# Optimization experiments

Hardware: AMD Instinct MI355X
Metric: run time of the kernel (lower is better)

The kernel has to match this reference:

```python
import jax, jax.numpy as jnp
import numpy as np

# dims (match init_kwargs / input_specs)
R, C, HD, D, K = 16, 64, 4, 16, 4   # num_rims, channels_per_rim, num_heads, depth, top_k
B, H, W = 8, 64, 64


def setup_inputs() -> dict:
    key = jax.random.key(0)
    ks = jax.random.split(key, 12)
    s = 0.02  # small init scale like torch conv default-ish
    OC = R * HD * D  # 1024
    return {
        "x":    jax.random.normal(ks[0], (B, C, H, W), jnp.float32),
        "rims": jax.random.normal(ks[1], (R, C), jnp.float32) * 0.01,  # spatial 1x1 squeezed
        "Wk":   jax.random.normal(ks[2], (OC, C), jnp.float32) * s,
        "bk":   jax.random.normal(ks[3], (OC,), jnp.float32) * s,
        "Wv":   jax.random.normal(ks[4], (OC, C), jnp.float32) * s,
        "bv":   jax.random.normal(ks[5], (OC,), jnp.float32) * s,
        "Wq":   jax.random.normal(ks[6], (OC, C), jnp.float32) * s,   # grouped conv, groups=R: (R, HD*D, C)
        "bq":   jax.random.normal(ks[7], (OC,), jnp.float32) * s,
        "Wm":   jax.random.normal(ks[8], (R * C, HD * D), jnp.float32) * s,  # merge heads, groups=R
        "bm":   jax.random.normal(ks[9], (R * C,), jnp.float32) * s,
        "Wo":   jax.random.normal(ks[10], (C, C), jnp.float32) * s,
        "bo":   jax.random.normal(ks[11], (C,), jnp.float32) * s,
    }


def reference(x, rims, Wk, bk, Wv, bv, Wq, bq, Wm, bm, Wo, bo):
    Bx, _, Hx, Wx = x.shape
    # input_key: cat(x, zeros) along batch, then 1x1 conv + relu -> [2B, R*HD*D, H, W]
    x2 = jnp.concatenate([x, jnp.zeros_like(x)], axis=0)
    keyf = jax.nn.relu(jnp.einsum('bchw,oc->bohw', x2, Wk) + bk[:, None, None])
    # input_value: 1x1 conv + relu -> [B, R*HD*D, H, W]
    val = jax.nn.relu(jnp.einsum('bchw,oc->bohw', x, Wv) + bv[:, None, None])
    # rims_query: grouped 1x1 conv over rims template -> [R, HD, D]
    q = jax.nn.relu(jnp.einsum('rc,rdc->rd', rims, Wq.reshape(R, HD * D, C))
                    + bq.reshape(R, HD * D)).reshape(R, HD, D)
    # attention inner product: grouped 1x1 conv (groups=R*HD) == per-(rim,head) dot over depth
    ip = jnp.einsum('brhdxy,rhd->brhxy', keyf.reshape(2 * Bx, R, HD, D, Hx, Wx), q)
    # softmax over the real-vs-null pair (dim 0 after split)
    attn = jax.nn.softmax(ip.reshape(2, Bx, R, HD, Hx, Wx), axis=0)
    attn_sum = attn.sum(axis=3)                 # [2, B, R, H, W]
    scores = jnp.moveaxis(attn_sum[0], 1, -1)   # [B, H, W, R]
    _, idx = jax.lax.top_k(scores, K)           # [B, H, W, K] (sorted)
    # merge heads: grouped 1x1 conv (groups=R) -> [B, R, C, H, W]
    merged = jnp.einsum('brdhw,rcd->brchw', val.reshape(Bx, R, HD * D, Hx, Wx),
                        Wm.reshape(R, C, HD * D)) \
             + bm.reshape(R, C)[None, :, :, None, None]
    # gather top-k rims per pixel, then mean over k
    idx2 = jnp.transpose(idx, (0, 3, 1, 2))[:, :, None, :, :]   # [B, K, 1, H, W]
    gathered = jnp.take_along_axis(merged, idx2, axis=1)        # [B, K, C, H, W]
    out = gathered.mean(axis=1)                                 # dropout(eval) = identity
    out = jax.nn.relu(out)
    # out projection: 1x1 conv + relu
    out = jax.nn.relu(jnp.einsum('bchw,oc->bohw', out, Wo) + bo[:, None, None])
    return out
```

## Files before the change

### kernel.cpp

```cpp
#include <hip/hip_runtime.h>
#include <math.h>

#define RN   16
#define CN   64
#define HDN  4
#define DN   16
#define KN   4
#define HWN  4096
#define NPIX 32768
#define OCN  1024
#define CHW  (CN*HWN)

__global__ __launch_bounds__(256) void rims_fused(
    const float* __restrict__ x,   const float* __restrict__ rims,
    const float* __restrict__ Wk,  const float* __restrict__ bk,
    const float* __restrict__ Wv,  const float* __restrict__ bv,
    const float* __restrict__ Wq,  const float* __restrict__ bq,
    const float* __restrict__ Wm,  const float* __restrict__ bm,
    const float* __restrict__ Wo,  const float* __restrict__ bo,
    float* __restrict__ out)
{
  __shared__ float q_s[OCN];
  __shared__ float ipn_s[64];
  __shared__ float sc_s[16 * 65];
  __shared__ float macc_s[64 * 65];
  __shared__ int   bcnt[16];
  __shared__ int   bpos[16];
  __shared__ unsigned char brim[256];
  __shared__ unsigned char bpix[256];

  const int tid   = threadIdx.x;
  const int tile  = blockIdx.x;
  const int b     = tile >> 6;
  const int pbase = (tile & 63) * 64;
  const float* xbase = x + (size_t)b * CHW + pbase;

  for (int o = tid; o < OCN; o += 256) {
    const int r = o >> 6;
    const float* wq = Wq + o * CN;
    const float* rp = rims + r * CN;
    float a0 = bq[o], a1 = 0.f, a2 = 0.f, a3 = 0.f;
    #pragma unroll
    for (int c = 0; c < CN; c += 4) {
      a0 = fmaf(wq[c+0], rp[c+0], a0);
      a1 = fmaf(wq[c+1], rp[c+1], a1);
      a2 = fmaf(wq[c+2], rp[c+2], a2);
      a3 = fmaf(wq[c+3], rp[c+3], a3);
    }
    q_s[o] = fmaxf((a0 + a1) + (a2 + a3), 0.f);
  }
  __syncthreads();
  if (tid < 64) {
    float acc = 0.f;
    #pragma unroll
    for (int d = 0; d < DN; ++d)
      acc = fmaf(fmaxf(bk[tid * DN + d], 0.f), q_s[tid * DN + d], acc);
    ipn_s[tid] = acc;
  }
  __syncthreads();

  {
    const int pl = tid & 63;
    const int g  = tid >> 6;
    const float* xp = xbase + pl;
    float xv[CN];
    #pragma unroll
    for (int c = 0; c < CN; ++c) xv[c] = xp[c * HWN];

    #pragma unroll 1
    for (int rr = 0; rr < 4; ++rr) {
      const int r = g * 4 + rr;
      float score = 0.f;
      #pragma unroll 1
      for (int h = 0; h < HDN; ++h) {
        const int rh = r * HDN + h;
        float qrow[DN];
        #pragma unroll
        for (int d = 0; d < DN; ++d) qrow[d] = q_s[rh * DN + d];
        const float ipn = ipn_s[rh];
        float ip = 0.f;
        #pragma unroll 1
        for (int d = 0; d < DN; ++d) {
          const float qv = qrow[d];
          if (qv != 0.f) {
            const int o = rh * DN + d;
            const float* w = Wk + o * CN;
            float a0 = bk[o], a1 = 0.f, a2 = 0.f, a3 = 0.f;
            #pragma unroll
            for (int c = 0; c < CN; c += 4) {
              a0 = fmaf(w[c+0], xv[c+0], a0);
              a1 = fmaf(w[c+1], xv[c+1], a1);
              a2 = fmaf(w[c+2], xv[c+2], a2);
              a3 = fmaf(w[c+3], xv[c+3], a3);
            }
            ip = fmaf(fmaxf((a0 + a1) + (a2 + a3), 0.f), qv, ip);
          }
        }
        score += 1.f / (1.f + expf(ipn - ip));
      }
      sc_s[r * 65 + pl] = score;
    }
  }
  __syncthreads();

  for (int i = tid; i < 64 * 65; i += 256) macc_s[i] = 0.f;
  if (tid < 16) bcnt[tid] = 0;
  __syncthreads();

  int rs0 = 0, rs1 = 0, rs2 = 0, rs3 = 0;
  if (tid < 64) {
    float s[RN];
    #pragma unroll
    for (int r = 0; r < RN; ++r) s[r] = sc_s[r * 65 + tid];
    #pragma unroll
    for (int k = 0; k < KN; ++k) {
      float best = -3.4e38f; int bi = 0;
      #pragma unroll
      for (int r = 0; r < RN; ++r) { if (s[r] > best) { best = s[r]; bi = r; } }
      if (k == 0) rs0 = bi; else if (k == 1) rs1 = bi;
      else if (k == 2) rs2 = bi; else rs3 = bi;
      s[bi] = -3.4e38f;
    }
    atomicAdd(&bcnt[rs0], 1); atomicAdd(&bcnt[rs1], 1);
    atomicAdd(&bcnt[rs2], 1); atomicAdd(&bcnt[rs3], 1);
  }
  __syncthreads();
  if (tid == 0) {
    int run = 0;
    #pragma unroll
    for (int r = 0; r < RN; ++r) { bpos[r] = run; run += bcnt[r]; }
  }
  __syncthreads();
  if (tid < 64) {
    int p0 = atomicAdd(&bpos[rs0], 1); brim[p0] = (unsigned char)rs0; bpix[p0] = (unsigned char)tid;
    int p1 = atomicAdd(&bpos[rs1], 1); brim[p1] = (unsigned char)rs1; bpix[p1] = (unsigned char)tid;
    int p2 = atomicAdd(&bpos[rs2], 1); brim[p2] = (unsigned char)rs2; bpix[p2] = (unsigned char)tid;
    int p3 = atomicAdd(&bpos[rs3], 1); brim[p3] = (unsigned char)rs3; bpix[p3] = (unsigned char)tid;
  }
  __syncthreads();

  {
    const int rim = (int)brim[tid];
    const int pp  = (int)bpix[tid];
    const float* xp = xbase + pp;
    float xv[CN];
    #pragma unroll
    for (int c = 0; c < CN; ++c) xv[c] = xp[c * HWN];

    float macc[CN];
    const float* bmp = bm + rim * CN;
    #pragma unroll
    for (int c = 0; c < CN; ++c) macc[c] = bmp[c];

    const float* wvb = Wv + (size_t)(rim * 64) * CN;
    const float* bvp = bv + rim * 64;
    const float* wmb = Wm + (size_t)(rim * CN) * 64;

    #pragma unroll 1
    for (int d0 = 0; d0 < 64; d0 += 8) {
      float vald[8];
      #pragma unroll
      for (int k8 = 0; k8 < 8; ++k8) {
        const int d = d0 + k8;
        const float* w = wvb + d * CN;
        float a0 = bvp[d], a1 = 0.f, a2 = 0.f, a3 = 0.f;
        #pragma unroll
        for (int c = 0; c < CN; c += 4) {
          a0 = fmaf(w[c+0], xv[c+0], a0);
          a1 = fmaf(w[c+1], xv[c+1], a1);
          a2 = fmaf(w[c+2], xv[c+2], a2);
          a3 = fmaf(w[c+3], xv[c+3], a3);
        }
        vald[k8] = fmaxf((a0 + a1) + (a2 + a3), 0.f);
      }
      #pragma unroll
      for (int c = 0; c < CN; ++c) {
        const float* wm = wmb + c * 64 + d0;
        float m = macc[c];
        #pragma unroll
        for (int k8 = 0; k8 < 8; ++k8) m = fmaf(wm[k8], vald[k8], m);
        macc[c] = m;
      }
    }
    #pragma unroll
    for (int c = 0; c < CN; ++c)
      atomicAdd(&macc_s[pp * 65 + c], macc[c]);
  }
  __syncthreads();

  {
    const int j  = tid >> 6;
    const int pl = tid & 63;
    float u[CN];
    #pragma unroll
    for (int c = 0; c < CN; ++c)
      u[c] = fmaxf(macc_s[pl * 65 + c] * 0.25f, 0.f);
    float* op = out + (size_t)b * CHW + pbase + pl;
    #pragma unroll 1
    for (int t = 0; t < 16; ++t) {
      const int co = j * 16 + t;
      const float* w = Wo + co * CN;
      float a0 = bo[co], a1 = 0.f, a2 = 0.f, a3 = 0.f;
      #pragma unroll
      for (int c = 0; c < CN; c += 4) {
        a0 = fmaf(w[c+0], u[c+0], a0);
        a1 = fmaf(w[c+1], u[c+1], a1);
        a2 = fmaf(w[c+2], u[c+2], a2);
        a3 = fmaf(w[c+3], u[c+3], a3);
      }
      op[co * HWN] = fmaxf((a0 + a1) + (a2 + a3), 0.f);
    }
  }
}

extern "C" void kernel_launch(void* const* d_in, const int* in_sizes, int n_in,
                              void* d_out, int out_size, void* d_ws, size_t ws_size,
                              hipStream_t stream) {
  (void)in_sizes; (void)n_in; (void)d_ws; (void)ws_size; (void)out_size;
  const float* xx   = (const float*)d_in[0];
  const float* rims = (const float*)d_in[1];
  const float* Wk   = (const float*)d_in[2];
  const float* bk   = (const float*)d_in[3];
  const float* Wv   = (const float*)d_in[4];
  const float* bv   = (const float*)d_in[5];
  const float* Wq   = (const float*)d_in[6];
  const float* bq   = (const float*)d_in[7];
  const float* Wm   = (const float*)d_in[8];
  const float* bm   = (const float*)d_in[9];
  const float* Wo   = (const float*)d_in[10];
  const float* bo   = (const float*)d_in[11];
  float* outp = (float*)d_out;

  rims_fused<<<dim3(NPIX / 64), dim3(256), 0, stream>>>(
      xx, rims, Wk, bk, Wv, bv, Wq, bq, Wm, bm, Wo, bo, outp);
}
```

Before: 398.3 us.

## Double block to 512 threads, compact active key channels, split merge work per pair

```diff
diff --git a/kernel.cpp b/kernel.cpp
--- a/kernel.cpp
+++ b/kernel.cpp
@@ -11,7 +11,7 @@
 #define OCN  1024
 #define CHW  (CN*HWN)
 
-__global__ __launch_bounds__(256) void rims_fused(
+__global__ __launch_bounds__(512, 4) void rims_fused(
     const float* __restrict__ x,   const float* __restrict__ rims,
     const float* __restrict__ Wk,  const float* __restrict__ bk,
     const float* __restrict__ Wv,  const float* __restrict__ bv,
@@ -22,6 +22,9 @@
 {
   __shared__ float q_s[OCN];
   __shared__ float ipn_s[64];
+  __shared__ float act_qv[64][16];
+  __shared__ int   act_o[64][16];
+  __shared__ int   act_cnt[64];
   __shared__ float sc_s[16 * 65];
   __shared__ float macc_s[64 * 65];
   __shared__ int   bcnt[16];
@@ -35,7 +38,17 @@
   const int pbase = (tile & 63) * 64;
   const float* xbase = x + (size_t)b * CHW + pbase;
 
-  for (int o = tid; o < OCN; o += 256) {
+  const int pl = tid & 63;
+  const int wv = tid >> 6;
+
+  float xv[CN];
+  {
+    const float* xp = xbase + pl;
+    #pragma unroll
+    for (int c = 0; c < CN; ++c) xv[c] = xp[c * HWN];
+  }
+
+  for (int o = tid; o < OCN; o += 512) {
     const int r = o >> 6;
     const float* wq = Wq + o * CN;
     const float* rp = rims + r * CN;
@@ -51,119 +64,35 @@
   }
   __syncthreads();
   if (tid < 64) {
-    float acc = 0.f;
-    #pragma unroll
-    for (int d = 0; d < DN; ++d)
-      acc = fmaf(fmaxf(bk[tid * DN + d], 0.f), q_s[tid * DN + d], acc);
-    ipn_s[tid] = acc;
-  }
-  __syncthreads();
-
-  {
-    const int pl = tid & 63;
-    const int g  = tid >> 6;
-    const float* xp = xbase + pl;
-    float xv[CN];
-    #pragma unroll
-    for (int c = 0; c < CN; ++c) xv[c] = xp[c * HWN];
-
+    int cnt = 0; float acc = 0.f;
+    #pragma unroll
+    for (int d = 0; d < DN; ++d) {
+      const int o = tid * DN + d;
+      const float qv = q_s[o];
+      acc = fmaf(fmaxf(bk[o], 0.f), qv, acc);
+      if (qv != 0.f) { act_o[tid][cnt] = o; act_qv[tid][cnt] = qv; ++cnt; }
+    }
+    ipn_s[tid]   = acc;
+    act_cnt[tid] = cnt;
+  }
+  __syncthreads();
+
+  #pragma unroll 1
+  for (int rr = 0; rr < 2; ++rr) {
+    const int r = wv * 2 + rr;
+    float score = 0.f;
     #pragma unroll 1
-    for (int rr = 0; rr < 4; ++rr) {
-      const int r = g * 4 + rr;
-      float score = 0.f;
-      #pragma unroll 1
-      for (int h = 0; h < HDN; ++h) {
-        const int rh = r * HDN + h;
-        float qrow[DN];
-        #pragma unroll
-        for (int d = 0; d < DN; ++d) qrow[d] = q_s[rh * DN + d];
-        const float ipn = ipn_s[rh];
-        float ip = 0.f;
-        #pragma unroll 1
-        for (int d = 0; d < DN; ++d) {
-          const float qv = qrow[d];
-          if (qv != 0.f) {
-            const int o = rh * DN + d;
-            const float* w = Wk + o * CN;
-            float a0 = bk[o], a1 = 0.f, a2 = 0.f, a3 = 0.f;
-            #pragma unroll
-            for (int c = 0; c < CN; c += 4) {
-              a0 = fmaf(w[c+0], xv[c+0], a0);
-              a1 = fmaf(w[c+1], xv[c+1], a1);
-              a2 = fmaf(w[c+2], xv[c+2], a2);
-              a3 = fmaf(w[c+3], xv[c+3], a3);
-            }
-            ip = fmaf(fmaxf((a0 + a1) + (a2 + a3), 0.f), qv, ip);
-          }
-        }
-        score += 1.f / (1.f + expf(ipn - ip));
-      }
-      sc_s[r * 65 + pl] = score;
-    }
-  }
-  __syncthreads();
-
-  for (int i = tid; i < 64 * 65; i += 256) macc_s[i] = 0.f;
-  if (tid < 16) bcnt[tid] = 0;
-  __syncthreads();
-
-  int rs0 = 0, rs1 = 0, rs2 = 0, rs3 = 0;
-  if (tid < 64) {
-    float s[RN];
-    #pragma unroll
-    for (int r = 0; r < RN; ++r) s[r] = sc_s[r * 65 + tid];
-    #pragma unroll
-    for (int k = 0; k < KN; ++k) {
-      float best = -3.4e38f; int bi = 0;
-      #pragma unroll
-      for (int r = 0; r < RN; ++r) { if (s[r] > best) { best = s[r]; bi = r; } }
-      if (k == 0) rs0 = bi; else if (k == 1) rs1 = bi;
-      else if (k == 2) rs2 = bi; else rs3 = bi;
-      s[bi] = -3.4e38f;
-    }
-    atomicAdd(&bcnt[rs0], 1); atomicAdd(&bcnt[rs1], 1);
-    atomicAdd(&bcnt[rs2], 1); atomicAdd(&bcnt[rs3], 1);
-  }
-  __syncthreads();
-  if (tid == 0) {
-    int run = 0;
-    #pragma unroll
-    for (int r = 0; r < RN; ++r) { bpos[r] = run; run += bcnt[r]; }
-  }
-  __syncthreads();
-  if (tid < 64) {
-    int p0 = atomicAdd(&bpos[rs0], 1); brim[p0] = (unsigned char)rs0; bpix[p0] = (unsigned char)tid;
-    int p1 = atomicAdd(&bpos[rs1], 1); brim[p1] = (unsigned char)rs1; bpix[p1] = (unsigned char)tid;
-    int p2 = atomicAdd(&bpos[rs2], 1); brim[p2] = (unsigned char)rs2; bpix[p2] = (unsigned char)tid;
-    int p3 = atomicAdd(&bpos[rs3], 1); brim[p3] = (unsigned char)rs3; bpix[p3] = (unsigned char)tid;
-  }
-  __syncthreads();
-
-  {
-    const int rim = (int)brim[tid];
-    const int pp  = (int)bpix[tid];
-    const float* xp = xbase + pp;
-    float xv[CN];
-    #pragma unroll
-    for (int c = 0; c < CN; ++c) xv[c] = xp[c * HWN];
-
-    float macc[CN];
-    const float* bmp = bm + rim * CN;
-    #pragma unroll
-    for (int c = 0; c < CN; ++c) macc[c] = bmp[c];
-
-    const float* wvb = Wv + (size_t)(rim * 64) * CN;
-    const float* bvp = bv + rim * 64;
-    const float* wmb = Wm + (size_t)(rim * CN) * 64;
-
-    #pragma unroll 1
-    for (int d0 = 0; d0 < 64; d0 += 8) {
-      float vald[8];
-      #pragma unroll
-      for (int k8 = 0; k8 < 8; ++k8) {
-        const int d = d0 + k8;
-        const float* w = wvb + d * CN;
-        float a0 = bvp[d], a1 = 0.f, a2 = 0.f, a3 = 0.f;
+    for (int h = 0; h < HDN; ++h) {
+      const int rh  = r * HDN + h;
+      const int cnt = __builtin_amdgcn_readfirstlane(act_cnt[rh]);
+      const float ipn = ipn_s[rh];
+      float ip = 0.f;
+      #pragma unroll 2
+      for (int i = 0; i < cnt; ++i) {
+        const int   o  = __builtin_amdgcn_readfirstlane(act_o[rh][i]);
+        const float qv = act_qv[rh][i];
+        const float* w = Wk + o * CN;
+        float a0 = bk[o], a1 = 0.f, a2 = 0.f, a3 = 0.f;
         #pragma unroll
         for (int c = 0; c < CN; c += 4) {
           a0 = fmaf(w[c+0], xv[c+0], a0);
@@ -171,34 +100,110 @@
           a2 = fmaf(w[c+2], xv[c+2], a2);
           a3 = fmaf(w[c+3], xv[c+3], a3);
         }
-        vald[k8] = fmaxf((a0 + a1) + (a2 + a3), 0.f);
-      }
-      #pragma unroll
-      for (int c = 0; c < CN; ++c) {
-        const float* wm = wmb + c * 64 + d0;
-        float m = macc[c];
-        #pragma unroll
-        for (int k8 = 0; k8 < 8; ++k8) m = fmaf(wm[k8], vald[k8], m);
-        macc[c] = m;
-      }
-    }
-    #pragma unroll
-    for (int c = 0; c < CN; ++c)
-      atomicAdd(&macc_s[pp * 65 + c], macc[c]);
+        ip = fmaf(fmaxf((a0 + a1) + (a2 + a3), 0.f), qv, ip);
+      }
+      score += 1.f / (1.f + expf(ipn - ip));
+    }
+    sc_s[r * 65 + pl] = score;
+  }
+  __syncthreads();
+
+  for (int i = tid; i < 64 * 65; i += 512) macc_s[i] = 0.f;
+  if (tid < 16) bcnt[tid] = 0;
+  __syncthreads();
+
+  int rs0 = 0, rs1 = 0, rs2 = 0, rs3 = 0;
+  if (tid < 64) {
+    float s[RN];
+    #pragma unroll
+    for (int r = 0; r < RN; ++r) s[r] = sc_s[r * 65 + tid];
+    #pragma unroll
+    for (int k = 0; k < KN; ++k) {
+      float best = -3.4e38f; int bi = 0;
+      #pragma unroll
+      for (int r = 0; r < RN; ++r) { if (s[r] > best) { best = s[r]; bi = r; } }
+      if (k == 0) rs0 = bi; else if (k == 1) rs1 = bi;
+      else if (k == 2) rs2 = bi; else rs3 = bi;
+      s[bi] = -3.4e38f;
+    }
+    atomicAdd(&bcnt[rs0], 1); atomicAdd(&bcnt[rs1], 1);
+    atomicAdd(&bcnt[rs2], 1); atomicAdd(&bcnt[rs3], 1);
+  }
+  __syncthreads();
+  if (tid == 0) {
+    int run = 0;
+    #pragma unroll
+    for (int r = 0; r < RN; ++r) { bpos[r] = run; run += bcnt[r]; }
+  }
+  __syncthreads();
+  if (tid < 64) {
+    int p0 = atomicAdd(&bpos[rs0], 1); brim[p0] = (unsigned char)rs0; bpix[p0] = (unsigned char)tid;
+    int p1 = atomicAdd(&bpos[rs1], 1); brim[p1] = (unsigned char)rs1; bpix[p1] = (unsigned char)tid;
+    int p2 = atomicAdd(&bpos[rs2], 1); brim[p2] = (unsigned char)rs2; bpix[p2] = (unsigned char)tid;
+    int p3 = atomicAdd(&bpos[rs3], 1); brim[p3] = (unsigned char)rs3; bpix[p3] = (unsigned char)tid;
   }
   __syncthreads();
 
   {
-    const int j  = tid >> 6;
-    const int pl = tid & 63;
+    const int e    = tid >> 1;
+    const int half = tid & 1;
+    const int rim  = (int)brim[e];
+    const int pp   = (int)bpix[e];
+    const float* xp = xbase + pp;
+    float xw[CN];
+    #pragma unroll
+    for (int c = 0; c < CN; ++c) xw[c] = xp[c * HWN];
+
+    float vald[32];
+    const float* wvb = Wv + (size_t)(rim * CN + half * 32) * CN;
+    const float* bvp = bv + rim * CN + half * 32;
+    #pragma unroll 4
+    for (int d = 0; d < 32; ++d) {
+      const float4* w4 = (const float4*)(wvb + d * CN);
+      float a0 = bvp[d], a1 = 0.f, a2 = 0.f, a3 = 0.f;
+      #pragma unroll
+      for (int c4 = 0; c4 < 16; ++c4) {
+        const float4 wq = w4[c4];
+        a0 = fmaf(wq.x, xw[c4*4+0], a0);
+        a1 = fmaf(wq.y, xw[c4*4+1], a1);
+        a2 = fmaf(wq.z, xw[c4*4+2], a2);
+        a3 = fmaf(wq.w, xw[c4*4+3], a3);
+      }
+      vald[d] = fmaxf((a0 + a1) + (a2 + a3), 0.f);
+    }
+
+    const float* wmb = Wm + (size_t)rim * CN * 64 + half * 32;
+    const float* bmp = bm + rim * CN;
+    #pragma unroll 2
+    for (int c = 0; c < CN; ++c) {
+      const float4* w4 = (const float4*)(wmb + c * 64);
+      float m0 = (half == 0) ? bmp[c] : 0.f;
+      float m1 = 0.f, m2 = 0.f, m3 = 0.f;
+      #pragma unroll
+      for (int k4 = 0; k4 < 8; ++k4) {
+        const float4 wq = w4[k4];
+        m0 = fmaf(wq.x, vald[k4*4+0], m0);
+        m1 = fmaf(wq.y, vald[k4*4+1], m1);
+        m2 = fmaf(wq.z, vald[k4*4+2], m2);
+        m3 = fmaf(wq.w, vald[k4*4+3], m3);
+      }
+      float m = (m0 + m1) + (m2 + m3);
+      m += __shfl_xor(m, 1);
+      if ((c >> 5) == half)
+        atomicAdd(&macc_s[pp * 65 + c], m);
+    }
+  }
+  __syncthreads();
+
+  {
     float u[CN];
     #pragma unroll
     for (int c = 0; c < CN; ++c)
       u[c] = fmaxf(macc_s[pl * 65 + c] * 0.25f, 0.f);
     float* op = out + (size_t)b * CHW + pbase + pl;
     #pragma unroll 1
-    for (int t = 0; t < 16; ++t) {
-      const int co = j * 16 + t;
+    for (int t = 0; t < 8; ++t) {
+      const int co = wv * 8 + t;
       const float* w = Wo + co * CN;
       float a0 = bo[co], a1 = 0.f, a2 = 0.f, a3 = 0.f;
       #pragma unroll
@@ -231,6 +236,6 @@
   const float* bo   = (const float*)d_in[11];
   float* outp = (float*)d_out;
 
-  rims_fused<<<dim3(NPIX / 64), dim3(256), 0, stream>>>(
+  rims_fused<<<dim3(NPIX / 64), dim3(512), 0, stream>>>(
       xx, rims, Wk, bk, Wv, bv, Wq, bq, Wm, bm, Wo, bo, outp);
 }
```

After: 631.3 us. 58.5% more time.

## Split fused RIMs kernel into score, mask, per-rim accumulate, and output kernels

Applied to the files above, without the earlier changes.

```diff
diff --git a/kernel.cpp b/kernel.cpp
--- a/kernel.cpp
+++ b/kernel.cpp
@@ -11,32 +11,40 @@
 #define OCN  1024
 #define CHW  (CN*HWN)
 
-__global__ __launch_bounds__(256) void rims_fused(
+#define WS_SC_BYTES   (16 * NPIX * 4)
+#define WS_MASK_BYTES (NPIX * 4)
+
+__global__ __launch_bounds__(256) void k_scores(
     const float* __restrict__ x,   const float* __restrict__ rims,
     const float* __restrict__ Wk,  const float* __restrict__ bk,
-    const float* __restrict__ Wv,  const float* __restrict__ bv,
     const float* __restrict__ Wq,  const float* __restrict__ bq,
-    const float* __restrict__ Wm,  const float* __restrict__ bm,
-    const float* __restrict__ Wo,  const float* __restrict__ bo,
-    float* __restrict__ out)
-{
-  __shared__ float q_s[OCN];
-  __shared__ float ipn_s[64];
-  __shared__ float sc_s[16 * 65];
-  __shared__ float macc_s[64 * 65];
-  __shared__ int   bcnt[16];
-  __shared__ int   bpos[16];
-  __shared__ unsigned char brim[256];
-  __shared__ unsigned char bpix[256];
-
-  const int tid   = threadIdx.x;
-  const int tile  = blockIdx.x;
-  const int b     = tile >> 6;
-  const int pbase = (tile & 63) * 64;
+    float* __restrict__ sc)
+{
+  __shared__ float q_s[512];
+  __shared__ float ipn_s[32];
+
+  const int tid  = threadIdx.x;
+  const int blk  = blockIdx.x;
+  const int T    = blk >> 1;
+  const int half = blk & 1;
+  const int b     = T >> 6;
+  const int pbase = (T & 63) * 64;
   const float* xbase = x + (size_t)b * CHW + pbase;
 
-  for (int o = tid; o < OCN; o += 256) {
-    const int r = o >> 6;
+  const int pl = tid & 63;
+  const int wv = tid >> 6;
+
+  float xv[CN];
+  {
+    const float* xp = xbase + pl;
+    #pragma unroll
+    for (int c = 0; c < CN; ++c) xv[c] = xp[c * HWN];
+  }
+
+  for (int i = 0; i < 2; ++i) {
+    const int ol = i * 256 + tid;
+    const int o  = half * 512 + ol;
+    const int r  = o >> 6;
     const float* wq = Wq + o * CN;
     const float* rp = rims + r * CN;
     float a0 = bq[o], a1 = 0.f, a2 = 0.f, a3 = 0.f;
@@ -47,129 +55,147 @@
       a2 = fmaf(wq[c+2], rp[c+2], a2);
       a3 = fmaf(wq[c+3], rp[c+3], a3);
     }
-    q_s[o] = fmaxf((a0 + a1) + (a2 + a3), 0.f);
-  }
-  __syncthreads();
-  if (tid < 64) {
+    q_s[ol] = fmaxf((a0 + a1) + (a2 + a3), 0.f);
+  }
+  __syncthreads();
+  if (tid < 32) {
     float acc = 0.f;
+    const int rh = half * 32 + tid;
     #pragma unroll
     for (int d = 0; d < DN; ++d)
-      acc = fmaf(fmaxf(bk[tid * DN + d], 0.f), q_s[tid * DN + d], acc);
+      acc = fmaf(fmaxf(bk[rh * DN + d], 0.f), q_s[tid * DN + d], acc);
     ipn_s[tid] = acc;
   }
   __syncthreads();
 
-  {
-    const int pl = tid & 63;
-    const int g  = tid >> 6;
-    const float* xp = xbase + pl;
-    float xv[CN];
-    #pragma unroll
-    for (int c = 0; c < CN; ++c) xv[c] = xp[c * HWN];
-
+  #pragma unroll 1
+  for (int rr = 0; rr < 2; ++rr) {
+    const int rl = wv * 2 + rr;
+    const int r  = half * 8 + rl;
+    float score = 0.f;
     #pragma unroll 1
-    for (int rr = 0; rr < 4; ++rr) {
-      const int r = g * 4 + rr;
-      float score = 0.f;
-      #pragma unroll 1
-      for (int h = 0; h < HDN; ++h) {
-        const int rh = r * HDN + h;
-        float qrow[DN];
-        #pragma unroll
-        for (int d = 0; d < DN; ++d) qrow[d] = q_s[rh * DN + d];
-        const float ipn = ipn_s[rh];
-        float ip = 0.f;
-        #pragma unroll 1
-        for (int d = 0; d < DN; ++d) {
-          const float qv = qrow[d];
-          if (qv != 0.f) {
-            const int o = rh * DN + d;
-            const float* w = Wk + o * CN;
-            float a0 = bk[o], a1 = 0.f, a2 = 0.f, a3 = 0.f;
-            #pragma unroll
-            for (int c = 0; c < CN; c += 4) {
-              a0 = fmaf(w[c+0], xv[c+0], a0);
-              a1 = fmaf(w[c+1], xv[c+1], a1);
-              a2 = fmaf(w[c+2], xv[c+2], a2);
-              a3 = fmaf(w[c+3], xv[c+3], a3);
-            }
-            ip = fmaf(fmaxf((a0 + a1) + (a2 + a3), 0.f), qv, ip);
-          }
-        }
-        score += 1.f / (1.f + expf(ipn - ip));
-      }
-      sc_s[r * 65 + pl] = score;
-    }
-  }
-  __syncthreads();
-
-  for (int i = tid; i < 64 * 65; i += 256) macc_s[i] = 0.f;
-  if (tid < 16) bcnt[tid] = 0;
-  __syncthreads();
-
-  int rs0 = 0, rs1 = 0, rs2 = 0, rs3 = 0;
-  if (tid < 64) {
-    float s[RN];
-    #pragma unroll
-    for (int r = 0; r < RN; ++r) s[r] = sc_s[r * 65 + tid];
-    #pragma unroll
-    for (int k = 0; k < KN; ++k) {
-      float best = -3.4e38f; int bi = 0;
-      #pragma unroll
-      for (int r = 0; r < RN; ++r) { if (s[r] > best) { best = s[r]; bi = r; } }
-      if (k == 0) rs0 = bi; else if (k == 1) rs1 = bi;
-      else if (k == 2) rs2 = bi; else rs3 = bi;
-      s[bi] = -3.4e38f;
-    }
-    atomicAdd(&bcnt[rs0], 1); atomicAdd(&bcnt[rs1], 1);
-    atomicAdd(&bcnt[rs2], 1); atomicAdd(&bcnt[rs3], 1);
-  }
-  __syncthreads();
-  if (tid == 0) {
-    int run = 0;
-    #pragma unroll
-    for (int r = 0; r < RN; ++r) { bpos[r] = run; run += bcnt[r]; }
-  }
-  __syncthreads();
-  if (tid < 64) {
-    int p0 = atomicAdd(&bpos[rs0], 1); brim[p0] = (unsigned char)rs0; bpix[p0] = (unsigned char)tid;
-    int p1 = atomicAdd(&bpos[rs1], 1); brim[p1] = (unsigned char)rs1; bpix[p1] = (unsigned char)tid;
-    int p2 = atomicAdd(&bpos[rs2], 1); brim[p2] = (unsigned char)rs2; bpix[p2] = (unsigned char)tid;
-    int p3 = atomicAdd(&bpos[rs3], 1); brim[p3] = (unsigned char)rs3; bpix[p3] = (unsigned char)tid;
-  }
-  __syncthreads();
-
-  {
-    const int rim = (int)brim[tid];
-    const int pp  = (int)bpix[tid];
-    const float* xp = xbase + pp;
-    float xv[CN];
-    #pragma unroll
-    for (int c = 0; c < CN; ++c) xv[c] = xp[c * HWN];
-
-    float macc[CN];
-    const float* bmp = bm + rim * CN;
-    #pragma unroll
-    for (int c = 0; c < CN; ++c) macc[c] = bmp[c];
-
-    const float* wvb = Wv + (size_t)(rim * 64) * CN;
-    const float* bvp = bv + rim * 64;
-    const float* wmb = Wm + (size_t)(rim * CN) * 64;
-
-    #pragma unroll 1
-    for (int d0 = 0; d0 < 64; d0 += 8) {
-      float vald[8];
-      #pragma unroll
-      for (int k8 = 0; k8 < 8; ++k8) {
-        const int d = d0 + k8;
-        const float* w = wvb + d * CN;
-        float a0 = bvp[d], a1 = 0.f, a2 = 0.f, a3 = 0.f;
+    for (int h = 0; h < HDN; ++h) {
+      const int rhl  = rl * HDN + h;
+      const int rh_u = __builtin_amdgcn_readfirstlane(r * HDN + h);
+      const float ipn = ipn_s[rhl];
+      float ip = 0.f;
+      #pragma unroll 4
+      for (int d = 0; d < DN; ++d) {
+        const float qv = q_s[rhl * DN + d];
+        const int   o  = rh_u * DN + d;
+        const float* w = Wk + o * CN;
+        float a0 = bk[o], a1 = 0.f, a2 = 0.f, a3 = 0.f;
         #pragma unroll
         for (int c = 0; c < CN; c += 4) {
           a0 = fmaf(w[c+0], xv[c+0], a0);
           a1 = fmaf(w[c+1], xv[c+1], a1);
           a2 = fmaf(w[c+2], xv[c+2], a2);
           a3 = fmaf(w[c+3], xv[c+3], a3);
+        }
+        ip = fmaf(fmaxf((a0 + a1) + (a2 + a3), 0.f), qv, ip);
+      }
+      score += 1.f / (1.f + expf(ipn - ip));
+    }
+    sc[r * NPIX + T * 64 + pl] = score;
+  }
+}
+
+__global__ __launch_bounds__(256) void k_mask(
+    const float* __restrict__ sc, unsigned int* __restrict__ mask,
+    float4* __restrict__ U4)
+{
+  const int pix = blockIdx.x * 256 + threadIdx.x;
+  for (int i = pix; i < (CN * NPIX) / 4; i += NPIX)
+    U4[i] = make_float4(0.f, 0.f, 0.f, 0.f);
+
+  float s[RN];
+  #pragma unroll
+  for (int r = 0; r < RN; ++r) s[r] = sc[r * NPIX + pix];
+  unsigned int m = 0;
+  #pragma unroll
+  for (int k = 0; k < KN; ++k) {
+    float best = -3.4e38f; int bi = 0;
+    #pragma unroll
+    for (int r = 0; r < RN; ++r) { if (s[r] > best) { best = s[r]; bi = r; } }
+    m |= (1u << bi);
+    s[bi] = -3.4e38f;
+  }
+  mask[pix] = m;
+}
+
+__global__ __launch_bounds__(256) void k_rimacc(
+    const float* __restrict__ x,  const unsigned int* __restrict__ mask,
+    const float* __restrict__ Wv, const float* __restrict__ bv,
+    const float* __restrict__ Wm, const float* __restrict__ bm,
+    float* __restrict__ U)
+{
+  __shared__ unsigned short plist[512];
+  __shared__ int wcnt[8];
+  __shared__ int woff[9];
+
+  const int tid   = threadIdx.x;
+  const int rim   = blockIdx.x >> 6;
+  const int chunk = blockIdx.x & 63;
+  const int pix0  = chunk * 512;
+  const int b     = pix0 >> 12;
+  const int hw0   = pix0 & 4095;
+  const float* xb = x + (size_t)b * CHW + hw0;
+
+  const int lane = tid & 63;
+  const int w    = tid >> 6;
+  const int i0 = w * 64 + lane;
+  const int i1 = 256 + w * 64 + lane;
+  const bool s0 = (mask[pix0 + i0] >> rim) & 1u;
+  const bool s1 = (mask[pix0 + i1] >> rim) & 1u;
+  const unsigned long long v0 = __ballot(s0);
+  const unsigned long long v1 = __ballot(s1);
+  if (lane == 0) { wcnt[w] = __popcll(v0); wcnt[4 + w] = __popcll(v1); }
+  __syncthreads();
+  if (tid == 0) {
+    int run = 0;
+    #pragma unroll
+    for (int j = 0; j < 8; ++j) { woff[j] = run; run += wcnt[j]; }
+    woff[8] = run;
+  }
+  __syncthreads();
+  const unsigned long long below = (1ull << lane) - 1ull;
+  if (s0) plist[woff[w]     + __popcll(v0 & below)] = (unsigned short)i0;
+  if (s1) plist[woff[4 + w] + __popcll(v1 & below)] = (unsigned short)i1;
+  __syncthreads();
+  const int n = woff[8];
+
+  const float* wvb = Wv + (size_t)(rim * CN) * CN;
+  const float* bvp = bv + rim * CN;
+  const float* wmb = Wm + (size_t)rim * CN * 64;
+  const float* bmp = bm + rim * CN;
+
+  for (int e0 = 0; e0 < n; e0 += 256) {
+    const int e = e0 + tid;
+    const bool active = e < n;
+    const int pp = active ? (int)plist[e] : (int)plist[0];
+    const float* xp = xb + pp;
+    float xv[CN];
+    #pragma unroll
+    for (int c = 0; c < CN; ++c) xv[c] = xp[c * HWN];
+
+    float macc[CN];
+    #pragma unroll
+    for (int c = 0; c < CN; ++c) macc[c] = bmp[c];
+
+    #pragma unroll 1
+    for (int d0 = 0; d0 < CN; d0 += 8) {
+      float vald[8];
+      #pragma unroll
+      for (int k8 = 0; k8 < 8; ++k8) {
+        const int d = d0 + k8;
+        const float* wr = wvb + d * CN;
+        float a0 = bvp[d], a1 = 0.f, a2 = 0.f, a3 = 0.f;
+        #pragma unroll
+        for (int c = 0; c < CN; c += 4) {
+          a0 = fmaf(wr[c+0], xv[c+0], a0);
+          a1 = fmaf(wr[c+1], xv[c+1], a1);
+          a2 = fmaf(wr[c+2], xv[c+2], a2);
+          a3 = fmaf(wr[c+3], xv[c+3], a3);
         }
         vald[k8] = fmaxf((a0 + a1) + (a2 + a3), 0.f);
       }
@@ -182,41 +208,51 @@
         macc[c] = m;
       }
     }
-    #pragma unroll
-    for (int c = 0; c < CN; ++c)
-      atomicAdd(&macc_s[pp * 65 + c], macc[c]);
-  }
-  __syncthreads();
-
-  {
-    const int j  = tid >> 6;
-    const int pl = tid & 63;
-    float u[CN];
-    #pragma unroll
-    for (int c = 0; c < CN; ++c)
-      u[c] = fmaxf(macc_s[pl * 65 + c] * 0.25f, 0.f);
-    float* op = out + (size_t)b * CHW + pbase + pl;
-    #pragma unroll 1
-    for (int t = 0; t < 16; ++t) {
-      const int co = j * 16 + t;
-      const float* w = Wo + co * CN;
-      float a0 = bo[co], a1 = 0.f, a2 = 0.f, a3 = 0.f;
+    if (active) {
+      const int pg = pix0 + pp;
       #pragma unroll
-      for (int c = 0; c < CN; c += 4) {
-        a0 = fmaf(w[c+0], u[c+0], a0);
-        a1 = fmaf(w[c+1], u[c+1], a1);
-        a2 = fmaf(w[c+2], u[c+2], a2);
-        a3 = fmaf(w[c+3], u[c+3], a3);
-      }
-      op[co * HWN] = fmaxf((a0 + a1) + (a2 + a3), 0.f);
-    }
+      for (int c = 0; c < CN; ++c)
+        atomicAdd(&U[c * NPIX + pg], macc[c]);
+    }
+  }
+}
+
+__global__ __launch_bounds__(256) void k_out(
+    const float* __restrict__ U,  const float* __restrict__ Wo,
+    const float* __restrict__ bo, float* __restrict__ out)
+{
+  const int tid = threadIdx.x;
+  const int q   = blockIdx.x & 3;
+  const int pix = (blockIdx.x >> 2) * 256 + tid;
+  const int b   = pix >> 12;
+  const int hw  = pix & 4095;
+
+  float u[CN];
+  #pragma unroll
+  for (int c = 0; c < CN; ++c)
+    u[c] = fmaxf(U[c * NPIX + pix] * 0.25f, 0.f);
+
+  float* op = out + (size_t)b * CHW + hw;
+  #pragma unroll 1
+  for (int t = 0; t < 16; ++t) {
+    const int co = q * 16 + t;
+    const float* wr = Wo + co * CN;
+    float a0 = bo[co], a1 = 0.f, a2 = 0.f, a3 = 0.f;
+    #pragma unroll
+    for (int c = 0; c < CN; c += 4) {
+      a0 = fmaf(wr[c+0], u[c+0], a0);
+      a1 = fmaf(wr[c+1], u[c+1], a1);
+      a2 = fmaf(wr[c+2], u[c+2], a2);
+      a3 = fmaf(wr[c+3], u[c+3], a3);
+    }
+    op[co * HWN] = fmaxf((a0 + a1) + (a2 + a3), 0.f);
   }
 }
 
 extern "C" void kernel_launch(void* const* d_in, const int* in_sizes, int n_in,
                               void* d_out, int out_size, void* d_ws, size_t ws_size,
                               hipStream_t stream) {
-  (void)in_sizes; (void)n_in; (void)d_ws; (void)ws_size; (void)out_size;
+  (void)in_sizes; (void)n_in; (void)ws_size; (void)out_size;
   const float* xx   = (const float*)d_in[0];
   const float* rims = (const float*)d_in[1];
   const float* Wk   = (const float*)d_in[2];
@@ -231,6 +267,13 @@
   const float* bo   = (const float*)d_in[11];
   float* outp = (float*)d_out;
 
-  rims_fused<<<dim3(NPIX / 64), dim3(256), 0, stream>>>(
-      xx, rims, Wk, bk, Wv, bv, Wq, bq, Wm, bm, Wo, bo, outp);
-}
+  char* ws = (char*)d_ws;
+  float*        sc   = (float*)(ws);
+  unsigned int* mask = (unsigned int*)(ws + WS_SC_BYTES);
+  float*        U    = (float*)(ws + WS_SC_BYTES + WS_MASK_BYTES);
+
+  k_scores<<<dim3(1024), dim3(256), 0, stream>>>(xx, rims, Wk, bk, Wq, bq, sc);
+  k_mask  <<<dim3(128),  dim3(256), 0, stream>>>(sc, mask, (float4*)U);
+  k_rimacc<<<dim3(1024), dim3(256), 0, stream>>>(xx, mask, Wv, bv, Wm, bm, U);
+  k_out   <<<dim3(512),  dim3(256), 0, stream>>>(U, Wo, bo, outp);
+}
```

After: 653.2 us. 64.0% more time.
